# Performance work log

Measured on AMD Instinct MI355X. Metric: run time of the kernel, lower is better.

Reference implementation:

```python
import jax, jax.numpy as jnp
import numpy as np

N_NODES = 100000
N_EDGES = 1600000
DIM_IN = 128
DIM_OUT = 64


def _spmm(edge_row, edge_col, edge_vals, X):
    # DAD.mm(X): sparse COO [N,N] times dense [N,d]
    # gather source features, scale by edge value, scatter-add to rows
    msgs = edge_vals[:, None] * X[edge_col]          # [E, d]
    return jax.ops.segment_sum(msgs, edge_row, num_segments=N_NODES)


def setup_inputs() -> dict:
    key = jax.random.key(0)
    k1, k2, k3, k4, k5, k6 = jax.random.split(key, 6)
    X = jax.random.normal(k1, (N_NODES, DIM_IN), dtype=jnp.float32)
    W1 = jax.random.normal(k2, (DIM_IN, DIM_IN), dtype=jnp.float32) * (1.0 / np.sqrt(DIM_IN))
    W2 = jax.random.normal(k3, (DIM_OUT, DIM_IN), dtype=jnp.float32) * (1.0 / np.sqrt(DIM_IN))
    edge_vals = jax.random.uniform(k4, (N_EDGES,), dtype=jnp.float32)
    edge_row = jax.random.randint(k5, (N_EDGES,), 0, N_NODES, dtype=jnp.int32)
    edge_col = jax.random.randint(k6, (N_EDGES,), 0, N_NODES, dtype=jnp.int32)
    return {"X": X, "W1": W1, "W2": W2, "edge_vals": edge_vals,
            "edge_row": edge_row, "edge_col": edge_col}


def reference(X, W1, W2, edge_vals, edge_row, edge_col):
    # layer 1: tanh(fc1(DAD @ X)); nn.Linear(bias=False) is x @ W.T
    h = jnp.tanh(_spmm(edge_row, edge_col, edge_vals, X) @ W1.T)
    # layer 2: tanh(fc2(DAD @ h))
    out = jnp.tanh(_spmm(edge_row, edge_col, edge_vals, h) @ W2.T)
    return out
```

## Files before the change

### kernel.cpp

```cpp
#include <hip/hip_runtime.h>
#include <hip/hip_bf16.h>
#include <hip/hip_fp16.h>

#define N_NODES 100000
#define N_EDGES 1600000
#define DIM_IN 128
#define DIM_OUT 64

#define NB 391
#define NCHUNK 391
#define CHUNK 4096
#define BCAP 5120
#define EPCAP 6144

typedef unsigned int uint;
typedef unsigned short ushort;
typedef _Float16 half8 __attribute__((ext_vector_type(8)));
typedef float f32x4 __attribute__((ext_vector_type(4)));

__device__ inline ushort f2h(float f) {
    __half h = __float2half(f);
    return *reinterpret_cast<ushort*>(&h);
}


__global__ __launch_bounds__(256) void chunk_hist_kernel(const int* __restrict__ erow,
                                                         int* __restrict__ counts, int E) {
    __shared__ int hist[NB];
    const int t = threadIdx.x, c = blockIdx.x;
    for (int b = t; b < NB; b += 256) hist[b] = 0;
    __syncthreads();
    const int eb = c * CHUNK;
#pragma unroll
    for (int i = 0; i < CHUNK / 256; ++i) {
        int e = eb + i * 256 + t;
        if (e < E) atomicAdd(&hist[erow[e] >> 8], 1);
    }
    __syncthreads();
    for (int b = t; b < NB; b += 256) counts[b * NCHUNK + c] = hist[b];
}

__global__ __launch_bounds__(512) void bucket_scan_kernel(const int* __restrict__ counts,
                                                          int* __restrict__ offnb,
                                                          int* __restrict__ tot) {
    __shared__ int s[512];
    const int b = blockIdx.x, t = threadIdx.x;
    int v = (t < NCHUNK) ? counts[b * NCHUNK + t] : 0;
    s[t] = v;
    __syncthreads();
#pragma unroll
    for (int o = 1; o < 512; o <<= 1) {
        int x = s[t];
        int y = (t >= o) ? s[t - o] : 0;
        __syncthreads();
        s[t] = x + y;
        __syncthreads();
    }
    if (t < NCHUNK) offnb[b * NCHUNK + t] = s[t] - v;
    if (t == 511) tot[b] = s[511];
}

__global__ __launch_bounds__(512) void base_scan_kernel(const int* __restrict__ tot,
                                                        int* __restrict__ bbase) {
    __shared__ int s[512];
    const int t = threadIdx.x;
    int v = (t < NB) ? tot[t] : 0;
    s[t] = v;
    __syncthreads();
#pragma unroll
    for (int o = 1; o < 512; o <<= 1) {
        int x = s[t];
        int y = (t >= o) ? s[t - o] : 0;
        __syncthreads();
        s[t] = x + y;
        __syncthreads();
    }
    if (t < NB) bbase[t] = s[t] - v;
    if (t == 511) bbase[NB] = s[511];
}

__global__ __launch_bounds__(512) void coarse_scatter_kernel(const int* __restrict__ erow,
                                                             const int* __restrict__ ecol,
                                                             const float* __restrict__ eval,
                                                             const int* __restrict__ offnb,
                                                             const int* __restrict__ bbase,
                                                             uint* __restrict__ keyOut,
                                                             float* __restrict__ valOut, int E) {
    __shared__ int hist[NB];
    __shared__ int segOff[NB];
    __shared__ int localOff[NB];
    __shared__ int sc[512];
    __shared__ int idxL[CHUNK];
    __shared__ int gaddrL[CHUNK];

    const int t = threadIdx.x, c = blockIdx.x;
    for (int b = t; b < NB; b += 512) {
        hist[b] = 0;
        segOff[b] = bbase[b] + offnb[b * NCHUNK + c];
    }
    __syncthreads();
    const int eb = c * CHUNK;
    uint bq[CHUNK / 512];
#pragma unroll
    for (int i = 0; i < CHUNK / 512; ++i) {
        int e = eb + i * 512 + t;
        if (e < E) {
            int b = erow[e] >> 8;
            int q = atomicAdd(&hist[b], 1);
            bq[i] = ((uint)b << 16) | (uint)q;
        } else {
            bq[i] = 0xFFFFFFFFu;
        }
    }
    __syncthreads();
    int v = (t < NB) ? hist[t] : 0;
    sc[t] = v;
    __syncthreads();
#pragma unroll
    for (int o = 1; o < 512; o <<= 1) {
        int x = sc[t];
        int y = (t >= o) ? sc[t - o] : 0;
        __syncthreads();
        sc[t] = x + y;
        __syncthreads();
    }
    if (t < NB) localOff[t] = sc[t] - v;
    __syncthreads();
#pragma unroll
    for (int i = 0; i < CHUNK / 512; ++i) {
        if (bq[i] != 0xFFFFFFFFu) {
            int b = bq[i] >> 16;
            int q = bq[i] & 0xFFFF;
            int s = localOff[b] + q;
            idxL[s] = eb + i * 512 + t;
            gaddrL[s] = segOff[b] + q;
        }
    }
    __syncthreads();
    const int m = min(CHUNK, E - eb);
    for (int s = t; s < m; s += 512) {
        int e = idxL[s];
        int g = gaddrL[s];
        keyOut[g] = ((uint)(erow[e] & 255) << 17) | (uint)ecol[e];
        valOut[g] = eval[e];
    }
}

__global__ __launch_bounds__(256) void fine_sort_kernel(const uint* __restrict__ keyOut,
                                                        const float* __restrict__ valOut,
                                                        const int* __restrict__ bbase,
                                                        int* __restrict__ row_ptr,
                                                        int* __restrict__ row_len,
                                                        int2* __restrict__ ep) {
    __shared__ uint keyL[BCAP];
    __shared__ int hist[256];
    __shared__ int offs[256];
    const int b = blockIdx.x, t = threadIdx.x;
    const int s0 = bbase[b], s1 = bbase[b + 1];
    const int m = min(s1 - s0, BCAP);
    hist[t] = 0;
    __syncthreads();
    for (int j = t; j < m; j += 256) {
        uint k = keyOut[s0 + j];
        keyL[j] = k;
        atomicAdd(&hist[k >> 17], 1);
    }
    __syncthreads();
    const int deg = hist[t];
    const int pdeg = (deg + 7) & ~7;
    offs[t] = pdeg;
    __syncthreads();
#pragma unroll
    for (int o = 1; o < 256; o <<= 1) {
        int x = offs[t];
        int y = (t >= o) ? offs[t - o] : 0;
        __syncthreads();
        offs[t] = x + y;
        __syncthreads();
    }
    const int pexcl = offs[t] - pdeg;
    const int base = b * EPCAP;
    const int row = b * 256 + t;
    if (row < N_NODES) {
        row_ptr[row] = base + pexcl;
        row_len[row] = pdeg;
    }
    hist[t] = pexcl;
    __syncthreads();
    for (int j = t; j < m; j += 256) {
        uint k = keyL[j];
        int pos = atomicAdd(&hist[k >> 17], 1);
        ep[base + pos] = make_int2((int)(k & 0x1FFFFu), __float_as_int(valOut[s0 + j]));
    }
    __syncthreads();
    for (int j = pexcl + deg; j < pexcl + pdeg; ++j)
        ep[base + j] = make_int2(0, 0);
}


__global__ __launch_bounds__(256) void cvt_weights_kernel(const float* __restrict__ W1,
                                                          const float* __restrict__ W2,
                                                          uint* __restrict__ W1h,
                                                          uint* __restrict__ W2h) {
    int i = blockIdx.x * 256 + threadIdx.x;
    const float* in;
    uint* outp;
    int j;
    if (i < 2048) { in = W1; outp = W1h; j = i; }
    else if (i < 3072) { in = W2; outp = W2h; j = i - 2048; }
    else return;
    const float4* in4 = reinterpret_cast<const float4*>(in) + (size_t)j * 2;
    float4 a = in4[0];
    float4 b = in4[1];
    uint4 o;
    o.x = (uint)f2h(a.x) | ((uint)f2h(a.y) << 16);
    o.y = (uint)f2h(a.z) | ((uint)f2h(a.w) << 16);
    o.z = (uint)f2h(b.x) | ((uint)f2h(b.y) << 16);
    o.w = (uint)f2h(b.z) | ((uint)f2h(b.w) << 16);
    reinterpret_cast<uint4*>(outp)[j] = o;
}


__global__ __launch_bounds__(256) void mfma_gemm128_kernel(const float* __restrict__ Af,
                                                           const uint* __restrict__ Wh,
                                                           uint* __restrict__ Out, int M) {
    __shared__ __align__(16) ushort sA[128 * 128];
    __shared__ __align__(16) ushort sB[128 * 128];

    const int t = threadIdx.x;
    const int l = t & 63;
    const int w = t >> 6;
    const int row0 = blockIdx.x * 128;
    const int lr = l & 15;
    const int lk = l >> 4;

#pragma unroll
    for (int i = 0; i < 16; ++i) {
        int fid = i * 256 + t;
        int row = fid >> 5, q4 = fid & 31;
        int gr = row0 + row;
        float4 v = make_float4(0.f, 0.f, 0.f, 0.f);
        if (gr < M) v = *reinterpret_cast<const float4*>(Af + (size_t)gr * 128 + q4 * 4);
        uint2 p;
        p.x = (uint)f2h(v.x) | ((uint)f2h(v.y) << 16);
        p.y = (uint)f2h(v.z) | ((uint)f2h(v.w) << 16);
        int slot = q4 >> 1;
        *reinterpret_cast<uint2*>(&sA[row * 128 + ((slot ^ (row & 7)) << 3) + (q4 & 1) * 4]) = p;
    }
#pragma unroll
    for (int i = 0; i < 8; ++i) {
        int fid = i * 256 + t;
        int row = fid >> 4, slot = fid & 15;
        uint4 v = reinterpret_cast<const uint4*>(Wh)[row * 16 + slot];
        *reinterpret_cast<uint4*>(&sB[row * 128 + ((slot ^ (row & 7)) << 3)]) = v;
    }
    __syncthreads();

    f32x4 acc[2][8];
#pragma unroll
    for (int rf = 0; rf < 2; ++rf)
#pragma unroll
        for (int cf = 0; cf < 8; ++cf) acc[rf][cf] = (f32x4){0.f, 0.f, 0.f, 0.f};

    half8 aF[2][4];
#pragma unroll
    for (int rf = 0; rf < 2; ++rf) {
        int row = w * 32 + rf * 16 + lr;
#pragma unroll
        for (int kc = 0; kc < 4; ++kc) {
            int slot = kc * 4 + lk;
            aF[rf][kc] = *reinterpret_cast<const half8*>(&sA[row * 128 + ((slot ^ (row & 7)) << 3)]);
        }
    }
#pragma unroll
    for (int cf = 0; cf < 8; ++cf) {
        int col = cf * 16 + lr;
#pragma unroll
        for (int kc = 0; kc < 4; ++kc) {
            int slot = kc * 4 + lk;
            half8 bF = *reinterpret_cast<const half8*>(&sB[col * 128 + ((slot ^ (col & 7)) << 3)]);
            acc[0][cf] = __builtin_amdgcn_mfma_f32_16x16x32_f16(aF[0][kc], bF, acc[0][cf], 0, 0, 0);
            acc[1][cf] = __builtin_amdgcn_mfma_f32_16x16x32_f16(aF[1][kc], bF, acc[1][cf], 0, 0, 0);
        }
    }
    __syncthreads();

    ushort* sOut = sA;
#pragma unroll
    for (int rf = 0; rf < 2; ++rf)
#pragma unroll
        for (int cf = 0; cf < 8; ++cf)
#pragma unroll
            for (int reg = 0; reg < 4; ++reg) {
                int row = w * 32 + rf * 16 + lk * 4 + reg;
                int col = cf * 16 + lr;
                sOut[row * 128 + col] = f2h(acc[rf][cf][reg]);
            }
    __syncthreads();
#pragma unroll
    for (int i = 0; i < 8; ++i) {
        int fid = i * 256 + t;
        int row = fid >> 4, q = fid & 15;
        int gr = row0 + row;
        if (gr < M)
            reinterpret_cast<uint4*>(Out)[(size_t)gr * 16 + q] =
                *reinterpret_cast<const uint4*>(&sOut[row * 128 + q * 8]);
    }
}


__global__ __launch_bounds__(256) void spmm1_fused_kernel(const int2* __restrict__ ep,
                                                          const int* __restrict__ row_ptr,
                                                          const int* __restrict__ row_len,
                                                          const uint* __restrict__ T,
                                                          const uint* __restrict__ W2h,
                                                          uint* __restrict__ Ph, int M) {
    __shared__ __align__(16) ushort sH[16 * 128];
    __shared__ __align__(16) ushort sW2[64 * 128];
    __shared__ __align__(16) ushort sP[16 * 64];

    const int t = threadIdx.x;
    const int l = t & 63;
    const int w = t >> 6;
    const int lr = l & 15;
    const int lk = l >> 4;
    const int row0 = blockIdx.x * 16;

#pragma unroll
    for (int i = 0; i < 4; ++i) {
        int fid = i * 256 + t;
        int row = fid >> 4, slot = fid & 15;
        uint4 v = reinterpret_cast<const uint4*>(W2h)[row * 16 + slot];
        *reinterpret_cast<uint4*>(&sW2[row * 128 + ((slot ^ (row & 7)) << 3)]) = v;
    }

    uint* sHu = reinterpret_cast<uint*>(sH);
#pragma unroll
    for (int rr = 0; rr < 4; ++rr) {
        const int lrow = w * 4 + rr;
        const int r = row0 + lrow;
        float a0x = 0.f, a0y = 0.f, a1x = 0.f, a1y = 0.f;
        if (r < M) {
            int beg = row_ptr[r];
            int end = beg + row_len[r];
            for (int e = beg; e < end; e += 8) {
                int2 cv[8];
                uint xu[8];
#pragma unroll
                for (int i = 0; i < 8; ++i) cv[i] = ep[e + i];
#pragma unroll
                for (int i = 0; i < 8; ++i) xu[i] = T[(size_t)cv[i].x * 64 + l];
#pragma unroll
                for (int i = 0; i < 8; ++i) {
                    float v = __int_as_float(cv[i].y);
                    __half2 h2 = *reinterpret_cast<__half2*>(&xu[i]);
                    float2 f = __half22float2(h2);
                    if (i & 1) { a1x += v * f.x; a1y += v * f.y; }
                    else       { a0x += v * f.x; a0y += v * f.y; }
                }
            }
        }
        uint hv = (uint)f2h(tanhf(a0x + a1x)) | ((uint)f2h(tanhf(a0y + a1y)) << 16);
        int slot = l >> 2;
        sHu[lrow * 64 + ((slot ^ (lrow & 7)) << 2) + (l & 3)] = hv;
    }
    __syncthreads();

    f32x4 acc = (f32x4){0.f, 0.f, 0.f, 0.f};
    const int col = w * 16 + lr;
#pragma unroll
    for (int kc = 0; kc < 4; ++kc) {
        int slot = kc * 4 + lk;
        half8 aF = *reinterpret_cast<const half8*>(&sH[lr * 128 + ((slot ^ (lr & 7)) << 3)]);
        half8 bF = *reinterpret_cast<const half8*>(&sW2[col * 128 + ((slot ^ (col & 7)) << 3)]);
        acc = __builtin_amdgcn_mfma_f32_16x16x32_f16(aF, bF, acc, 0, 0, 0);
    }
#pragma unroll
    for (int reg = 0; reg < 4; ++reg) {
        int row = lk * 4 + reg;
        sP[row * 64 + col] = f2h(acc[reg]);
    }
    __syncthreads();

    if (t < 128) {
        int row = t >> 3, q = t & 7;
        int gr = row0 + row;
        if (gr < M)
            reinterpret_cast<uint4*>(Ph)[(size_t)gr * 8 + q] =
                *reinterpret_cast<const uint4*>(&sP[row * 64 + q * 8]);
    }
}


__global__ __launch_bounds__(256) void spmm2_kernel(const int2* __restrict__ ep,
                                                    const int* __restrict__ row_ptr,
                                                    const int* __restrict__ row_len,
                                                    const ushort* __restrict__ Ph,
                                                    float* __restrict__ out) {
    int wave = threadIdx.x >> 6;
    int lane = threadIdx.x & 63;
    int r = blockIdx.x * 4 + wave;
    if (r >= N_NODES) return;
    int beg = row_ptr[r];
    int end = beg + row_len[r];
    float acc0 = 0.f, acc1 = 0.f;
    for (int e = beg; e < end; e += 8) {
        int2 cv[8];
        ushort xu[8];
#pragma unroll
        for (int i = 0; i < 8; ++i) cv[i] = ep[e + i];
#pragma unroll
        for (int i = 0; i < 8; ++i) xu[i] = Ph[(size_t)cv[i].x * 64 + lane];
#pragma unroll
        for (int i = 0; i < 8; ++i) {
            float v = __int_as_float(cv[i].y);
            __half h = *reinterpret_cast<__half*>(&xu[i]);
            float x = __half2float(h);
            if (i & 1) acc1 += v * x;
            else       acc0 += v * x;
        }
    }
    out[(size_t)r * DIM_OUT + lane] = tanhf(acc0 + acc1);
}


extern "C" void kernel_launch(void* const* d_in, const int* in_sizes, int n_in,
                              void* d_out, int out_size, void* d_ws, size_t ws_size,
                              hipStream_t stream) {
    const float* X = (const float*)d_in[0];
    const float* W1 = (const float*)d_in[1];
    const float* W2 = (const float*)d_in[2];
    const float* evals = (const float*)d_in[3];
    const int* erow = (const int*)d_in[4];
    const int* ecol = (const int*)d_in[5];
    float* out = (float*)d_out;

    const int N = N_NODES;
    const int E = N_EDGES;

    char* ws = (char*)d_ws;
    size_t off = 0;
    auto alloc = [&](size_t bytes) {
        size_t o = off;
        off = (off + bytes + 255) & ~(size_t)255;
        return o;
    };
    size_t o_counts = alloc((size_t)NB * NCHUNK * 4);
    size_t o_offnb = alloc((size_t)NB * NCHUNK * 4);
    size_t o_tot = alloc((size_t)NB * 4);
    size_t o_bbase = alloc((size_t)(NB + 1) * 4);
    size_t o_rowptr = alloc((size_t)N * 4);
    size_t o_rowlen = alloc((size_t)N * 4);
    size_t o_ep = alloc((size_t)NB * EPCAP * 8);
    size_t o_key = alloc((size_t)E * 4);
    size_t o_val = alloc((size_t)E * 4);
    size_t o_xw1 = alloc((size_t)N * 64 * 4);
    size_t o_ph = alloc((size_t)N * 32 * 4);
    size_t o_w1h = alloc((size_t)128 * 64 * 4);
    size_t o_w2h = alloc((size_t)64 * 64 * 4);
    (void)ws_size;

    int* counts = (int*)(ws + o_counts);
    int* offnb = (int*)(ws + o_offnb);
    int* tot = (int*)(ws + o_tot);
    int* bbase = (int*)(ws + o_bbase);
    int* row_ptr = (int*)(ws + o_rowptr);
    int* row_len = (int*)(ws + o_rowlen);
    int2* ep = (int2*)(ws + o_ep);
    uint* keyOut = (uint*)(ws + o_key);
    float* valOut = (float*)(ws + o_val);
    uint* XW1h = (uint*)(ws + o_xw1);
    uint* Ph = (uint*)(ws + o_ph);
    uint* W1h = (uint*)(ws + o_w1h);
    uint* W2h = (uint*)(ws + o_w2h);

    const int gemm_grid = (N + 127) / 128;
    const int spmm2_grid = (N + 3) / 4;
    const int fused_grid = (N + 15) / 16;

    cvt_weights_kernel<<<12, 256, 0, stream>>>(W1, W2, W1h, W2h);
    mfma_gemm128_kernel<<<gemm_grid, 256, 0, stream>>>(X, W1h, XW1h, N);

    chunk_hist_kernel<<<NCHUNK, 256, 0, stream>>>(erow, counts, E);
    bucket_scan_kernel<<<NB, 512, 0, stream>>>(counts, offnb, tot);
    base_scan_kernel<<<1, 512, 0, stream>>>(tot, bbase);
    coarse_scatter_kernel<<<NCHUNK, 512, 0, stream>>>(erow, ecol, evals, offnb, bbase,
                                                      keyOut, valOut, E);
    fine_sort_kernel<<<NB, 256, 0, stream>>>(keyOut, valOut, bbase, row_ptr, row_len, ep);

    spmm1_fused_kernel<<<fused_grid, 256, 0, stream>>>(ep, row_ptr, row_len, XW1h, W2h, Ph, N);
    spmm2_kernel<<<spmm2_grid, 256, 0, stream>>>(ep, row_ptr, row_len, (const ushort*)Ph, out);
}
```

Baseline: 200.0 us.

## Balance SpMM1 edge work across waves via row-tagged edges and LDS atomics

```diff
diff --git a/kernel.cpp b/kernel.cpp
--- a/kernel.cpp
+++ b/kernel.cpp
@@ -12,6 +12,7 @@
 #define CHUNK 4096
 #define BCAP 5120
 #define EPCAP 6144
+#define SACC_STRIDE 136
 
 typedef unsigned int uint;
 typedef unsigned short ushort;
@@ -189,12 +190,14 @@
     __syncthreads();
     for (int j = t; j < m; j += 256) {
         uint k = keyL[j];
-        int pos = atomicAdd(&hist[k >> 17], 1);
-        ep[base + pos] = make_int2((int)(k & 0x1FFFFu), __float_as_int(valOut[s0 + j]));
+        int r8 = (int)(k >> 17);
+        int pos = atomicAdd(&hist[r8], 1);
+        ep[base + pos] = make_int2((int)(((uint)(r8 & 15) << 17) | (k & 0x1FFFFu)),
+                                   __float_as_int(valOut[s0 + j]));
     }
     __syncthreads();
     for (int j = pexcl + deg; j < pexcl + pdeg; ++j)
-        ep[base + j] = make_int2(0, 0);
+        ep[base + j] = make_int2((int)((uint)(t & 15) << 17), 0);
 }
 
 
@@ -315,8 +318,8 @@
                                                           const uint* __restrict__ T,
                                                           const uint* __restrict__ W2h,
                                                           uint* __restrict__ Ph, int M) {
+    __shared__ float sAcc[16 * SACC_STRIDE];
     __shared__ __align__(16) ushort sH[16 * 128];
-    __shared__ __align__(16) ushort sW2[64 * 128];
     __shared__ __align__(16) ushort sP[16 * 64];
 
     const int t = threadIdx.x;
@@ -326,43 +329,56 @@
     const int lk = l >> 4;
     const int row0 = blockIdx.x * 16;
 
-#pragma unroll
-    for (int i = 0; i < 4; ++i) {
-        int fid = i * 256 + t;
-        int row = fid >> 4, slot = fid & 15;
-        uint4 v = reinterpret_cast<const uint4*>(W2h)[row * 16 + slot];
-        *reinterpret_cast<uint4*>(&sW2[row * 128 + ((slot ^ (row & 7)) << 3)]) = v;
-    }
-
-    uint* sHu = reinterpret_cast<uint*>(sH);
-#pragma unroll
-    for (int rr = 0; rr < 4; ++rr) {
-        const int lrow = w * 4 + rr;
-        const int r = row0 + lrow;
-        float a0x = 0.f, a0y = 0.f, a1x = 0.f, a1y = 0.f;
-        if (r < M) {
-            int beg = row_ptr[r];
-            int end = beg + row_len[r];
-            for (int e = beg; e < end; e += 8) {
-                int2 cv[8];
-                uint xu[8];
-#pragma unroll
-                for (int i = 0; i < 8; ++i) cv[i] = ep[e + i];
-#pragma unroll
-                for (int i = 0; i < 8; ++i) xu[i] = T[(size_t)cv[i].x * 64 + l];
-#pragma unroll
-                for (int i = 0; i < 8; ++i) {
-                    float v = __int_as_float(cv[i].y);
-                    __half2 h2 = *reinterpret_cast<__half2*>(&xu[i]);
-                    float2 f = __half22float2(h2);
-                    if (i & 1) { a1x += v * f.x; a1y += v * f.y; }
-                    else       { a0x += v * f.x; a0y += v * f.y; }
-                }
+    for (int i = t; i < 16 * SACC_STRIDE; i += 256) sAcc[i] = 0.f;
+    __syncthreads();
+
+    const int bbeg = row_ptr[row0];
+    const int bend = row_ptr[row0 + 15] + row_len[row0 + 15];
+    const int nb = (bend - bbeg) >> 3;
+    const int b0 = (nb * w) >> 2;
+    const int b1 = (nb * (w + 1)) >> 2;
+
+    int cur = -1;
+    float a0x = 0.f, a0y = 0.f, a1x = 0.f, a1y = 0.f;
+    for (int bi = b0; bi < b1; ++bi) {
+        const int e = bbeg + bi * 8;
+        int2 cv[8];
+#pragma unroll
+        for (int i = 0; i < 8; ++i) cv[i] = ep[e + i];
+        const int row = cv[0].x >> 17;
+        uint xu[8];
+#pragma unroll
+        for (int i = 0; i < 8; ++i) xu[i] = T[(size_t)(cv[i].x & 0x1FFFF) * 64 + l];
+        if (row != cur) {
+            if (cur >= 0) {
+                atomicAdd(&sAcc[cur * SACC_STRIDE + 2 * l], a0x + a1x);
+                atomicAdd(&sAcc[cur * SACC_STRIDE + 2 * l + 1], a0y + a1y);
             }
-        }
-        uint hv = (uint)f2h(tanhf(a0x + a1x)) | ((uint)f2h(tanhf(a0y + a1y)) << 16);
-        int slot = l >> 2;
-        sHu[lrow * 64 + ((slot ^ (lrow & 7)) << 2) + (l & 3)] = hv;
+            cur = row;
+            a0x = a0y = a1x = a1y = 0.f;
+        }
+#pragma unroll
+        for (int i = 0; i < 8; ++i) {
+            float v = __int_as_float(cv[i].y);
+            __half2 h2 = *reinterpret_cast<__half2*>(&xu[i]);
+            float2 f = __half22float2(h2);
+            if (i & 1) { a1x += v * f.x; a1y += v * f.y; }
+            else       { a0x += v * f.x; a0y += v * f.y; }
+        }
+    }
+    if (cur >= 0) {
+        atomicAdd(&sAcc[cur * SACC_STRIDE + 2 * l], a0x + a1x);
+        atomicAdd(&sAcc[cur * SACC_STRIDE + 2 * l + 1], a0y + a1y);
+    }
+    __syncthreads();
+
+    {
+        const int row = t & 15, slot = t >> 4;
+        half8 h;
+#pragma unroll
+        for (int j = 0; j < 8; ++j)
+            h[j] = (_Float16)tanhf(sAcc[row * SACC_STRIDE + slot * 8 + j]);
+        *reinterpret_cast<half8*>(&sH[row * 128 + ((slot ^ (row & 7)) << 3)]) = h;
     }
     __syncthreads();
 
@@ -370,24 +386,21 @@
     const int col = w * 16 + lr;
 #pragma unroll
     for (int kc = 0; kc < 4; ++kc) {
-        int slot = kc * 4 + lk;
+        const int slot = kc * 4 + lk;
         half8 aF = *reinterpret_cast<const half8*>(&sH[lr * 128 + ((slot ^ (lr & 7)) << 3)]);
-        half8 bF = *reinterpret_cast<const half8*>(&sW2[col * 128 + ((slot ^ (col & 7)) << 3)]);
+        const uint4 wv = reinterpret_cast<const uint4*>(W2h)[col * 16 + slot];
+        half8 bF = *reinterpret_cast<const half8*>(&wv);
         acc = __builtin_amdgcn_mfma_f32_16x16x32_f16(aF, bF, acc, 0, 0, 0);
     }
 #pragma unroll
-    for (int reg = 0; reg < 4; ++reg) {
-        int row = lk * 4 + reg;
-        sP[row * 64 + col] = f2h(acc[reg]);
-    }
+    for (int reg = 0; reg < 4; ++reg)
+        sP[(lk * 4 + reg) * 64 + col] = f2h(acc[reg]);
     __syncthreads();
 
     if (t < 128) {
-        int row = t >> 3, q = t & 7;
-        int gr = row0 + row;
-        if (gr < M)
-            reinterpret_cast<uint4*>(Ph)[(size_t)gr * 8 + q] =
-                *reinterpret_cast<const uint4*>(&sP[row * 64 + q * 8]);
+        const int row = t >> 3, q = t & 7;
+        reinterpret_cast<uint4*>(Ph)[(size_t)(row0 + row) * 8 + q] =
+            *reinterpret_cast<const uint4*>(&sP[row * 64 + q * 8]);
     }
 }
 
@@ -410,7 +423,7 @@
 #pragma unroll
         for (int i = 0; i < 8; ++i) cv[i] = ep[e + i];
 #pragma unroll
-        for (int i = 0; i < 8; ++i) xu[i] = Ph[(size_t)cv[i].x * 64 + lane];
+        for (int i = 0; i < 8; ++i) xu[i] = Ph[(size_t)(cv[i].x & 0x1FFFF) * 64 + lane];
 #pragma unroll
         for (int i = 0; i < 8; ++i) {
             float v = __int_as_float(cv[i].y);
@@ -476,7 +489,7 @@
 
     const int gemm_grid = (N + 127) / 128;
     const int spmm2_grid = (N + 3) / 4;
-    const int fused_grid = (N + 15) / 16;
+    const int fused_grid = N / 16;
 
     cvt_weights_kernel<<<12, 256, 0, stream>>>(W1, W2, W1h, W2h);
     mfma_gemm128_kernel<<<gemm_grid, 256, 0, stream>>>(X, W1h, XW1h, N);
```

Measured after the change: 233.1 us. +16.5%, slower.
